# Kernel optimization log

Hardware: AMD Instinct MI355X
Metric: run time of the kernel (lower is better)

## Reference

```python
import jax, jax.numpy as jnp
import numpy as np

D_MODEL = 1024
N_HEAD = 16
B, C, S = 4, 4, 1024


def setup_inputs() -> dict:
    key = jax.random.key(0)
    ks = jax.random.split(key, 5)
    d = D_MODEL
    x = jax.random.normal(ks[0], (B, C, S, d), dtype=jnp.float32)
    scale = 1.0 / np.sqrt(d).astype(np.float32)

    def lin(k):
        return jax.random.normal(k, (d, d), dtype=jnp.float32) * scale

    return {
        "x": x,
        "wq": lin(ks[1]), "bq": jnp.zeros((d,), jnp.float32),
        "wk": lin(ks[2]), "bk": jnp.zeros((d,), jnp.float32),
        "wv": lin(ks[3]), "bv": jnp.zeros((d,), jnp.float32),
        "wo": lin(ks[4]), "bo": jnp.zeros((d,), jnp.float32),
    }


def reference(x, wq, bq, wk, bk, wv, bv, wo, bo):
    b, c, s, d = x.shape
    dh = d // N_HEAD
    nh = N_HEAD * c  # channels folded into heads, as in torch .view

    def proj(w, bias):
        # nn.Linear: y = x @ w.T + b  (w stored as [out, in])
        y = jnp.einsum('bcsd,ed->bcse', x, w) + bias
        # view(B, -1, n_head*C, d_head).transpose(1, 2) -> (B, nh, S, dh)
        return jnp.swapaxes(y.reshape(b, -1, nh, dh), 1, 2)

    # NOTE: original multiplies query by sqrt(d_head) (kept faithfully)
    q = proj(wq, bq) * jnp.sqrt(jnp.asarray(dh, x.dtype))
    k = proj(wk, bk)
    v = proj(wv, bv)

    attn = jax.nn.softmax(jnp.einsum('bhqd,bhkd->bhqk', q, k), axis=-1)
    o = jnp.einsum('bhqk,bhkd->bhqd', attn, v)          # (B, nh, S, dh)
    o = jnp.swapaxes(o, 1, 2).reshape(b, -1, N_HEAD * dh)  # (B, S*C, d)
    o = jnp.einsum('bnd,ed->bne', o, wo) + bo
    return o.reshape(b, c, -1, d)  # (B, C, S, d)
```

## Files before the change

### kernel.cpp

```cpp
#include <hip/hip_runtime.h>
#include <stdint.h>

typedef unsigned short u16;
typedef _Float16 f16;
typedef __attribute__((ext_vector_type(8))) _Float16 f16x8;
typedef __attribute__((ext_vector_type(4))) float f32x4;

__device__ __forceinline__ float exp2fast(float x) {
  return __builtin_amdgcn_exp2f(x);
}

__device__ __forceinline__ f32x4 mfma16(f16x8 a, f16x8 b, f32x4 c) {
  return __builtin_amdgcn_mfma_f32_16x16x32_f16(a, b, c, 0, 0, 0);
}

__device__ __forceinline__ u16 f2h(float f) {
  return __builtin_bit_cast(u16, (f16)f);
}

__device__ __forceinline__ void gld16(const void* g, void* l) {
  __builtin_amdgcn_global_load_lds(
      (const __attribute__((address_space(1))) unsigned int*)g,
      (__attribute__((address_space(3))) unsigned int*)l,
      16, 0, 0);
}

__global__ __launch_bounds__(256) void cvt_f32_f16(const float* __restrict__ in,
                                                   u16* __restrict__ out, int n4) {
  int stride = gridDim.x * blockDim.x;
  for (int i = blockIdx.x * blockDim.x + threadIdx.x; i < n4; i += stride) {
    float4 v = reinterpret_cast<const float4*>(in)[i];
    ushort4 o;
    o.x = f2h(v.x); o.y = f2h(v.y); o.z = f2h(v.z); o.w = f2h(v.w);
    reinterpret_cast<ushort4*>(out)[i] = o;
  }
}

struct Ptr8 {
  const float *s0, *s1, *s2, *s3;
  u16 *d0, *d1, *d2, *d3;
};
__global__ __launch_bounds__(256) void cvt4_f32_f16(Ptr8 p, int n4) {
  const float* in = (blockIdx.y == 0) ? p.s0 : (blockIdx.y == 1) ? p.s1
                    : (blockIdx.y == 2) ? p.s2 : p.s3;
  u16* out = (blockIdx.y == 0) ? p.d0 : (blockIdx.y == 1) ? p.d1
             : (blockIdx.y == 2) ? p.d2 : p.d3;
  int stride = gridDim.x * blockDim.x;
  for (int i = blockIdx.x * blockDim.x + threadIdx.x; i < n4; i += stride) {
    float4 v = reinterpret_cast<const float4*>(in)[i];
    ushort4 o;
    o.x = f2h(v.x); o.y = f2h(v.y); o.z = f2h(v.z); o.w = f2h(v.w);
    reinterpret_cast<ushort4*>(out)[i] = o;
  }
}

template <int ITERS>
__device__ __forceinline__ void stageR(const u16* __restrict__ M, int r0, int k0,
                                       u16* S, int wid, int lane) {
  const int l8 = lane >> 3;
  const int col = k0 + (((lane & 7) ^ l8) << 3);
#pragma unroll
  for (int it = 0; it < ITERS; ++it) {
    const int rowbase = wid * (ITERS * 8) + it * 8;
    gld16(M + (size_t)(r0 + rowbase + l8) * 1024 + col, S + rowbase * 64);
  }
}

__global__ __launch_bounds__(512) void proj_qkv(
    const u16* __restrict__ xb,
    const u16* __restrict__ wqh, const u16* __restrict__ wkh, const u16* __restrict__ wvh,
    const float* __restrict__ bq, const float* __restrict__ bk, const float* __restrict__ bv,
    u16* __restrict__ Qf, u16* __restrict__ Kf, u16* __restrict__ Vt) {
  const int mat = blockIdx.z;
  const u16* __restrict__ w = (mat == 0) ? wqh : (mat == 1) ? wkh : wvh;
  const float* __restrict__ bias = (mat == 0) ? bq : (mat == 1) ? bk : bv;
  const int m0 = blockIdx.x * 256;
  const int n0 = blockIdx.y * 128;

  __shared__ __align__(16) u16 As[256 * 64];
  __shared__ __align__(16) u16 Bs[128 * 64];

  const int tid = threadIdx.x;
  const int lane = tid & 63;
  const int wid = tid >> 6;
  const int wr = wid >> 1;
  const int wc = wid & 1;
  const int qd = lane >> 4, lm = lane & 15;

  f32x4 acc[4][4];
#pragma unroll
  for (int i = 0; i < 4; ++i)
#pragma unroll
    for (int j = 0; j < 4; ++j) acc[i][j] = (f32x4){0.f, 0.f, 0.f, 0.f};

  stageR<4>(xb, m0, 0, As, wid, lane);
  stageR<2>(w, n0, 0, Bs, wid, lane);

  for (int kt = 0; kt < 16; ++kt) {
    __syncthreads();
#pragma unroll
    for (int ks = 0; ks < 2; ++ks) {
      const int gofs = ((ks * 4 + qd) ^ (lm & 7)) << 3;
      f16x8 af[4], bf[4];
#pragma unroll
      for (int i = 0; i < 4; ++i)
        af[i] = *reinterpret_cast<const f16x8*>(As + (wr * 64 + i * 16 + lm) * 64 + gofs);
#pragma unroll
      for (int j = 0; j < 4; ++j)
        bf[j] = *reinterpret_cast<const f16x8*>(Bs + (wc * 64 + j * 16 + lm) * 64 + gofs);
#pragma unroll
      for (int i = 0; i < 4; ++i)
#pragma unroll
        for (int j = 0; j < 4; ++j)
          acc[i][j] = mfma16(af[i], bf[j], acc[i][j]);
    }
    __syncthreads();
    if (kt + 1 < 16) {
      stageR<4>(xb, m0, (kt + 1) * 64, As, wid, lane);
      stageR<2>(w, n0, (kt + 1) * 64, Bs, wid, lane);
    }
  }

  const float scale = (mat == 0) ? 11.5415603f : 1.0f;
#pragma unroll
  for (int i = 0; i < 4; ++i) {
#pragma unroll
    for (int r = 0; r < 4; ++r) {
      int R = m0 + wr * 64 + i * 16 + qd * 4 + r;
      int bb = R >> 12, n = R & 4095;
      int cc = n >> 10, s = n & 1023;
      int rb = s & 3, t = s >> 2;
      int m = cc * 256 + t;
#pragma unroll
      for (int j = 0; j < 4; ++j) {
        int e = n0 + wc * 64 + j * 16 + lm;
        int head = e >> 6, jj = e & 63;
        int h = rb * 16 + head;
        float val = (acc[i][j][r] + bias[e]) * scale;
        u16 hv = f2h(val);
        if (mat == 2) {
          Vt[(((size_t)bb * 64 + h) * 64 + jj) * 1024 + m] = hv;
        } else {
          size_t idx = (((size_t)bb * 64 + h) * 1024 + m) * 64 + jj;
          if (mat == 0) Qf[idx] = hv;
          else          Kf[idx] = hv;
        }
      }
    }
  }
}

__device__ __forceinline__ f16x8 lds_frag(const u16* base, int row, int blk) {
  return *reinterpret_cast<const f16x8*>(base + row * 64 + ((blk ^ (row & 7)) << 3));
}

__device__ __forceinline__ void stage_kv(const u16* __restrict__ Kh,
                                         const u16* __restrict__ Vh, int kc,
                                         u16* KsB, u16* VsB, int wv, int lane) {
  const int l8 = lane >> 3, sl = lane & 7;
  const int rb = wv * 16;
#pragma unroll
  for (int it = 0; it < 2; ++it) {
    int row = rb + it * 8 + l8;
    int gsl = sl ^ l8;
    gld16(Kh + (size_t)(kc * 64 + row) * 64 + gsl * 8, KsB + (rb + it * 8) * 64);
    gld16(Vh + (size_t)row * 1024 + kc * 64 + gsl * 8, VsB + (rb + it * 8) * 64);
  }
}

__global__ __launch_bounds__(256) void attn_kernel(
    const u16* __restrict__ Qf, const u16* __restrict__ Kf,
    const u16* __restrict__ Vt, u16* __restrict__ Of) {
  const int wgid = (blockIdx.x & 7) * 256 + (blockIdx.x >> 3);
  const int bh = wgid >> 3;
  const int m0 = (wgid & 7) * 128;
  const int b = bh >> 6, h = bh & 63;
  const int tid = threadIdx.x, lane = tid & 63, wv = tid >> 6;
  const int qd = lane >> 4, lm = lane & 15;

  __shared__ __align__(16) u16 Ks[2][64 * 64];
  __shared__ __align__(16) u16 Vs[2][64 * 64];

  const size_t hb = (size_t)(b * 64 + h);
  const u16* __restrict__ Qh = Qf + hb * 65536;
  const u16* __restrict__ Kh = Kf + hb * 65536;
  const u16* __restrict__ Vh = Vt + hb * 65536;

  f16x8 qf[2][2];
#pragma unroll
  for (int im = 0; im < 2; ++im)
#pragma unroll
    for (int ks = 0; ks < 2; ++ks)
      qf[im][ks] = *reinterpret_cast<const f16x8*>(
          Qh + (size_t)(m0 + wv * 32 + im * 16 + lm) * 64 + ks * 32 + qd * 8);

  f32x4 oa[2][4];
  float mrow[2] = {-1e30f, -1e30f};
  float lrow[2] = {0.f, 0.f};
#pragma unroll
  for (int im = 0; im < 2; ++im)
#pragma unroll
    for (int jf = 0; jf < 4; ++jf) oa[im][jf] = (f32x4){0.f, 0.f, 0.f, 0.f};

  stage_kv(Kh, Vh, 0, &Ks[0][0], &Vs[0][0], wv, lane);

  for (int kc = 0; kc < 16; ++kc) {
    const int buf = kc & 1;
    __syncthreads();
    if (kc + 1 < 16) stage_kv(Kh, Vh, kc + 1, &Ks[buf ^ 1][0], &Vs[buf ^ 1][0], wv, lane);

    f32x4 sc[2][4];
#pragma unroll
    for (int im = 0; im < 2; ++im)
#pragma unroll
      for (int nf = 0; nf < 4; ++nf) sc[im][nf] = (f32x4){0.f, 0.f, 0.f, 0.f};
    __builtin_amdgcn_s_setprio(1);
#pragma unroll
    for (int ks = 0; ks < 2; ++ks) {
      f16x8 kfr[4];
#pragma unroll
      for (int nf = 0; nf < 4; ++nf)
        kfr[nf] = lds_frag(&Ks[buf][0], nf * 16 + lm, ks * 4 + qd);
#pragma unroll
      for (int im = 0; im < 2; ++im)
#pragma unroll
        for (int nf = 0; nf < 4; ++nf)
          sc[im][nf] = mfma16(kfr[nf], qf[im][ks], sc[im][nf]);
    }
    __builtin_amdgcn_s_setprio(0);

    unsigned int pk[2][8];
#pragma unroll
    for (int im = 0; im < 2; ++im) {
      float pm = sc[im][0][0];
#pragma unroll
      for (int nf = 0; nf < 4; ++nf)
#pragma unroll
        for (int r = 0; r < 4; ++r) pm = fmaxf(pm, sc[im][nf][r]);
      pm = fmaxf(pm, __shfl_xor(pm, 16));
      pm = fmaxf(pm, __shfl_xor(pm, 32));
      if (__all(pm <= mrow[im] + 8.0f)) {
        float mn = mrow[im];
        float s = 0.f;
#pragma unroll
        for (int nf = 0; nf < 4; ++nf) {
          float p0 = exp2fast(sc[im][nf][0] - mn);
          float p1 = exp2fast(sc[im][nf][1] - mn);
          float p2 = exp2fast(sc[im][nf][2] - mn);
          float p3 = exp2fast(sc[im][nf][3] - mn);
          s += (p0 + p1) + (p2 + p3);
          pk[im][2 * nf + 0] = __builtin_bit_cast(unsigned int, __builtin_amdgcn_cvt_pkrtz(p0, p1));
          pk[im][2 * nf + 1] = __builtin_bit_cast(unsigned int, __builtin_amdgcn_cvt_pkrtz(p2, p3));
        }
        s += __shfl_xor(s, 16);
        s += __shfl_xor(s, 32);
        lrow[im] += s;
      } else {
        float mn = fmaxf(mrow[im], pm);
        float corr = exp2fast(mrow[im] - mn);
        mrow[im] = mn;
        float s = 0.f;
#pragma unroll
        for (int nf = 0; nf < 4; ++nf) {
          float p0 = exp2fast(sc[im][nf][0] - mn);
          float p1 = exp2fast(sc[im][nf][1] - mn);
          float p2 = exp2fast(sc[im][nf][2] - mn);
          float p3 = exp2fast(sc[im][nf][3] - mn);
          s += (p0 + p1) + (p2 + p3);
          pk[im][2 * nf + 0] = __builtin_bit_cast(unsigned int, __builtin_amdgcn_cvt_pkrtz(p0, p1));
          pk[im][2 * nf + 1] = __builtin_bit_cast(unsigned int, __builtin_amdgcn_cvt_pkrtz(p2, p3));
        }
        s += __shfl_xor(s, 16);
        s += __shfl_xor(s, 32);
        lrow[im] = lrow[im] * corr + s;
#pragma unroll
        for (int r = 0; r < 4; ++r) {
          float cb = __shfl(corr, qd * 4 + r);
#pragma unroll
          for (int jf = 0; jf < 4; ++jf) oa[im][jf][r] *= cb;
        }
      }
    }

#pragma unroll
    for (int ks = 0; ks < 2; ++ks) {
      f16x8 vfr[4];
#pragma unroll
      for (int jf = 0; jf < 4; ++jf)
        vfr[jf] = lds_frag(&Vs[buf][0], jf * 16 + lm, ks * 4 + qd);
#pragma unroll
      for (int im = 0; im < 2; ++im) {
        union { unsigned int w[4]; f16x8 hv; } pa;
#pragma unroll
        for (int w = 0; w < 4; ++w) {
          int srcl = (((2 * qd + (w >> 1)) & 3) << 4) + lm;
          unsigned int a0 = __shfl(pk[im][2 * (2 * ks + 0) + (w & 1)], srcl);
          unsigned int a1 = __shfl(pk[im][2 * (2 * ks + 1) + (w & 1)], srcl);
          pa.w[w] = (qd & 2) ? a1 : a0;
        }
        __builtin_amdgcn_s_setprio(1);
#pragma unroll
        for (int jf = 0; jf < 4; ++jf)
          oa[im][jf] = mfma16(pa.hv, vfr[jf], oa[im][jf]);
        __builtin_amdgcn_s_setprio(0);
      }
    }
  }

  const int rb = h >> 4, head = h & 15;
#pragma unroll
  for (int im = 0; im < 2; ++im) {
#pragma unroll
    for (int r = 0; r < 4; ++r) {
      float lb = __shfl(lrow[im], qd * 4 + r);
      float inv = 1.0f / lb;
      int mq = m0 + wv * 32 + im * 16 + qd * 4 + r;
      int c = mq >> 8, t = mq & 255;
      int s = t * 4 + rb;
      int n = c * 1024 + s;
#pragma unroll
      for (int jf = 0; jf < 4; ++jf) {
        int j = jf * 16 + lm;
        int f = head * 64 + j;
        Of[((size_t)b * 4096 + n) * 1024 + f] = f2h(oa[im][jf][r] * inv);
      }
    }
  }
}

__global__ __launch_bounds__(512) void out_gemm(
    const u16* __restrict__ Of, const u16* __restrict__ woh,
    const float* __restrict__ bo, float* __restrict__ out) {
  const int m0 = blockIdx.x * 256;
  const int n0 = blockIdx.y * 128;

  __shared__ __align__(16) u16 As[256 * 64];
  __shared__ __align__(16) u16 Bs[128 * 64];

  const int tid = threadIdx.x;
  const int lane = tid & 63;
  const int wid = tid >> 6;
  const int wr = wid >> 1, wc = wid & 1;
  const int qd = lane >> 4, lm = lane & 15;

  f32x4 acc[4][4];
#pragma unroll
  for (int i = 0; i < 4; ++i)
#pragma unroll
    for (int j = 0; j < 4; ++j) acc[i][j] = (f32x4){0.f, 0.f, 0.f, 0.f};

  stageR<4>(Of, m0, 0, As, wid, lane);
  stageR<2>(woh, n0, 0, Bs, wid, lane);

  for (int kt = 0; kt < 16; ++kt) {
    __syncthreads();
#pragma unroll
    for (int ks = 0; ks < 2; ++ks) {
      const int gofs = ((ks * 4 + qd) ^ (lm & 7)) << 3;
      f16x8 af[4], bf[4];
#pragma unroll
      for (int i = 0; i < 4; ++i)
        af[i] = *reinterpret_cast<const f16x8*>(As + (wr * 64 + i * 16 + lm) * 64 + gofs);
#pragma unroll
      for (int j = 0; j < 4; ++j)
        bf[j] = *reinterpret_cast<const f16x8*>(Bs + (wc * 64 + j * 16 + lm) * 64 + gofs);
#pragma unroll
      for (int i = 0; i < 4; ++i)
#pragma unroll
        for (int j = 0; j < 4; ++j)
          acc[i][j] = mfma16(af[i], bf[j], acc[i][j]);
    }
    __syncthreads();
    if (kt + 1 < 16) {
      stageR<4>(Of, m0, (kt + 1) * 64, As, wid, lane);
      stageR<2>(woh, n0, (kt + 1) * 64, Bs, wid, lane);
    }
  }

#pragma unroll
  for (int i = 0; i < 4; ++i) {
#pragma unroll
    for (int r = 0; r < 4; ++r) {
      int R = m0 + wr * 64 + i * 16 + qd * 4 + r;
#pragma unroll
      for (int j = 0; j < 4; ++j) {
        int e = n0 + wc * 64 + j * 16 + lm;
        out[(size_t)R * 1024 + e] = acc[i][j][r] + bo[e];
      }
    }
  }
}

extern "C" void kernel_launch(void* const* d_in, const int* in_sizes, int n_in,
                              void* d_out, int out_size, void* d_ws, size_t ws_size,
                              hipStream_t stream) {
  const float* x  = (const float*)d_in[0];
  const float* wq = (const float*)d_in[1];
  const float* bq = (const float*)d_in[2];
  const float* wk = (const float*)d_in[3];
  const float* bk = (const float*)d_in[4];
  const float* wv = (const float*)d_in[5];
  const float* bv = (const float*)d_in[6];
  const float* wo = (const float*)d_in[7];
  const float* bo = (const float*)d_in[8];
  float* out = (float*)d_out;

  char* ws = (char*)d_ws;
  u16* xb  = (u16*)(ws + 0);
  u16* wqh = (u16*)(ws + 33554432);
  u16* wkh = (u16*)(ws + 35651584);
  u16* wvh = (u16*)(ws + 37748736);
  u16* woh = (u16*)(ws + 39845888);
  u16* Qfb = (u16*)(ws + 41943040);
  u16* Kfb = (u16*)(ws + 75497472);
  u16* Vtb = (u16*)(ws + 109051904);
  u16* Ofb = (u16*)(ws + 142606336);

  cvt_f32_f16<<<4096, 256, 0, stream>>>(x, xb, 16777216 / 4);
  Ptr8 p { wq, wk, wv, wo, wqh, wkh, wvh, woh };
  cvt4_f32_f16<<<dim3(256, 4), 256, 0, stream>>>(p, 1048576 / 4);

  proj_qkv<<<dim3(64, 8, 3), 512, 0, stream>>>(xb, wqh, wkh, wvh, bq, bk, bv,
                                               Qfb, Kfb, Vtb);
  attn_kernel<<<2048, 256, 0, stream>>>(Qfb, Kfb, Vtb, Ofb);
  out_gemm<<<dim3(64, 8), 512, 0, stream>>>(Ofb, woh, bo, out);
}
```

Baseline: 382.4 us.

## Triple-buffer LDS GEMM mainloop with register ping-pong and explicit waitcnt barriers

Replaces the single-buffered, sync-heavy mainloop shared by the QKV projection and output GEMMs with a common helper. The helper keeps three LDS stages in flight using global_load_lds, splits each K-tile into two register fragment sets that alternate, and uses raw s_waitcnt/s_barrier plus s_setprio around the MFMA bursts. The aim is to overlap global-to-LDS traffic and LDS reads with matrix math instead of stalling on full syncs every tile. LDS per block roughly triples, which limits residency to about one block per CU despite the launch-bounds hint, and the hand-counted vmcnt values are fragile.

```diff
diff --git a/kernel.cpp b/kernel.cpp
--- a/kernel.cpp
+++ b/kernel.cpp
@@ -66,7 +66,81 @@
   }
 }
 
-__global__ __launch_bounds__(512) void proj_qkv(
+__device__ __forceinline__ void gemm8ph(
+    const u16* __restrict__ A, const u16* __restrict__ B,
+    int m0, int n0, u16* As, u16* Bs,
+    int wid, int lane, f32x4 (&acc)[4][4]) {
+  const int wr = wid >> 1, wc = wid & 1;
+  const int qd = lane >> 4, lm = lane & 15;
+  const int g0 = (qd ^ (lm & 7)) << 3;
+  const int g1 = ((4 + qd) ^ (lm & 7)) << 3;
+  const int arow = (wr * 64 + lm) * 64;
+  const int brow = (wc * 64 + lm) * 64;
+
+  stageR<4>(A, m0, 0,  As,         wid, lane);
+  stageR<2>(B, n0, 0,  Bs,         wid, lane);
+  stageR<4>(A, m0, 64, As + 16384, wid, lane);
+  stageR<2>(B, n0, 64, Bs + 8192,  wid, lane);
+  asm volatile("s_waitcnt vmcnt(6)\n\ts_barrier" ::: "memory");
+
+  f16x8 a0[4], b0[4], a1[4], b1[4];
+#pragma unroll
+  for (int i = 0; i < 4; ++i)
+    a0[i] = *reinterpret_cast<const f16x8*>(As + arow + i * 1024 + g0);
+#pragma unroll
+  for (int j = 0; j < 4; ++j)
+    b0[j] = *reinterpret_cast<const f16x8*>(Bs + brow + j * 1024 + g0);
+
+  int buf = 0, nb = 2;
+  for (int t = 0; t < 16; ++t) {
+    const u16* aB = As + buf * 16384;
+    const u16* bB = Bs + buf * 8192;
+    if (t < 14) stageR<4>(A, m0, (t + 2) * 64, As + nb * 16384, wid, lane);
+#pragma unroll
+    for (int i = 0; i < 4; ++i)
+      a1[i] = *reinterpret_cast<const f16x8*>(aB + arow + i * 1024 + g1);
+#pragma unroll
+    for (int j = 0; j < 4; ++j)
+      b1[j] = *reinterpret_cast<const f16x8*>(bB + brow + j * 1024 + g1);
+    asm volatile("s_barrier" ::: "memory");
+    __builtin_amdgcn_s_setprio(1);
+#pragma unroll
+    for (int i = 0; i < 4; ++i)
+#pragma unroll
+      for (int j = 0; j < 4; ++j)
+        acc[i][j] = mfma16(a0[i], b0[j], acc[i][j]);
+    __builtin_amdgcn_s_setprio(0);
+    asm volatile("s_barrier" ::: "memory");
+    if (t < 14) stageR<2>(B, n0, (t + 2) * 64, Bs + nb * 8192, wid, lane);
+    if (t < 15) {
+      if (t < 14) asm volatile("s_waitcnt vmcnt(6)\n\ts_barrier" ::: "memory");
+      else        asm volatile("s_waitcnt vmcnt(0)\n\ts_barrier" ::: "memory");
+      int b2 = buf + 1; if (b2 == 3) b2 = 0;
+      const u16* aN = As + b2 * 16384;
+      const u16* bN = Bs + b2 * 8192;
+#pragma unroll
+      for (int i = 0; i < 4; ++i)
+        a0[i] = *reinterpret_cast<const f16x8*>(aN + arow + i * 1024 + g0);
+#pragma unroll
+      for (int j = 0; j < 4; ++j)
+        b0[j] = *reinterpret_cast<const f16x8*>(bN + brow + j * 1024 + g0);
+    } else {
+      asm volatile("s_barrier" ::: "memory");
+    }
+    __builtin_amdgcn_s_setprio(1);
+#pragma unroll
+    for (int i = 0; i < 4; ++i)
+#pragma unroll
+      for (int j = 0; j < 4; ++j)
+        acc[i][j] = mfma16(a1[i], b1[j], acc[i][j]);
+    __builtin_amdgcn_s_setprio(0);
+    asm volatile("s_barrier" ::: "memory");
+    ++buf; if (buf == 3) buf = 0;
+    ++nb;  if (nb == 3)  nb = 0;
+  }
+}
+
+__global__ __launch_bounds__(512, 2) void proj_qkv(
     const u16* __restrict__ xb,
     const u16* __restrict__ wqh, const u16* __restrict__ wkh, const u16* __restrict__ wvh,
     const float* __restrict__ bq, const float* __restrict__ bk, const float* __restrict__ bv,
@@ -77,14 +151,13 @@
   const int m0 = blockIdx.x * 256;
   const int n0 = blockIdx.y * 128;
 
-  __shared__ __align__(16) u16 As[256 * 64];
-  __shared__ __align__(16) u16 Bs[128 * 64];
+  __shared__ __align__(16) u16 As[3 * 256 * 64];
+  __shared__ __align__(16) u16 Bs[3 * 128 * 64];
 
   const int tid = threadIdx.x;
   const int lane = tid & 63;
   const int wid = tid >> 6;
-  const int wr = wid >> 1;
-  const int wc = wid & 1;
+  const int wr = wid >> 1, wc = wid & 1;
   const int qd = lane >> 4, lm = lane & 15;
 
   f32x4 acc[4][4];
@@ -93,33 +166,7 @@
 #pragma unroll
     for (int j = 0; j < 4; ++j) acc[i][j] = (f32x4){0.f, 0.f, 0.f, 0.f};
 
-  stageR<4>(xb, m0, 0, As, wid, lane);
-  stageR<2>(w, n0, 0, Bs, wid, lane);
-
-  for (int kt = 0; kt < 16; ++kt) {
-    __syncthreads();
-#pragma unroll
-    for (int ks = 0; ks < 2; ++ks) {
-      const int gofs = ((ks * 4 + qd) ^ (lm & 7)) << 3;
-      f16x8 af[4], bf[4];
-#pragma unroll
-      for (int i = 0; i < 4; ++i)
-        af[i] = *reinterpret_cast<const f16x8*>(As + (wr * 64 + i * 16 + lm) * 64 + gofs);
-#pragma unroll
-      for (int j = 0; j < 4; ++j)
-        bf[j] = *reinterpret_cast<const f16x8*>(Bs + (wc * 64 + j * 16 + lm) * 64 + gofs);
-#pragma unroll
-      for (int i = 0; i < 4; ++i)
-#pragma unroll
-        for (int j = 0; j < 4; ++j)
-          acc[i][j] = mfma16(af[i], bf[j], acc[i][j]);
-    }
-    __syncthreads();
-    if (kt + 1 < 16) {
-      stageR<4>(xb, m0, (kt + 1) * 64, As, wid, lane);
-      stageR<2>(w, n0, (kt + 1) * 64, Bs, wid, lane);
-    }
-  }
+  gemm8ph(xb, w, m0, n0, As, Bs, wid, lane, acc);
 
   const float scale = (mat == 0) ? 11.5415603f : 1.0f;
 #pragma unroll
@@ -328,14 +375,14 @@
   }
 }
 
-__global__ __launch_bounds__(512) void out_gemm(
+__global__ __launch_bounds__(512, 2) void out_gemm(
     const u16* __restrict__ Of, const u16* __restrict__ woh,
     const float* __restrict__ bo, float* __restrict__ out) {
   const int m0 = blockIdx.x * 256;
   const int n0 = blockIdx.y * 128;
 
-  __shared__ __align__(16) u16 As[256 * 64];
-  __shared__ __align__(16) u16 Bs[128 * 64];
+  __shared__ __align__(16) u16 As[3 * 256 * 64];
+  __shared__ __align__(16) u16 Bs[3 * 128 * 64];
 
   const int tid = threadIdx.x;
   const int lane = tid & 63;
@@ -349,33 +396,7 @@
 #pragma unroll
     for (int j = 0; j < 4; ++j) acc[i][j] = (f32x4){0.f, 0.f, 0.f, 0.f};
 
-  stageR<4>(Of, m0, 0, As, wid, lane);
-  stageR<2>(woh, n0, 0, Bs, wid, lane);
-
-  for (int kt = 0; kt < 16; ++kt) {
-    __syncthreads();
-#pragma unroll
-    for (int ks = 0; ks < 2; ++ks) {
-      const int gofs = ((ks * 4 + qd) ^ (lm & 7)) << 3;
-      f16x8 af[4], bf[4];
-#pragma unroll
-      for (int i = 0; i < 4; ++i)
-        af[i] = *reinterpret_cast<const f16x8*>(As + (wr * 64 + i * 16 + lm) * 64 + gofs);
-#pragma unroll
-      for (int j = 0; j < 4; ++j)
-        bf[j] = *reinterpret_cast<const f16x8*>(Bs + (wc * 64 + j * 16 + lm) * 64 + gofs);
-#pragma unroll
-      for (int i = 0; i < 4; ++i)
-#pragma unroll
-        for (int j = 0; j < 4; ++j)
-          acc[i][j] = mfma16(af[i], bf[j], acc[i][j]);
-    }
-    __syncthreads();
-    if (kt + 1 < 16) {
-      stageR<4>(Of, m0, (kt + 1) * 64, As, wid, lane);
-      stageR<2>(woh, n0, (kt + 1) * 64, Bs, wid, lane);
-    }
-  }
+  gemm8ph(Of, woh, m0, n0, As, Bs, wid, lane, acc);
 
 #pragma unroll
   for (int i = 0; i < 4; ++i) {
```

Result: slower. 437.3 us (+14.4%).
